# Performance work log

Measured on AMD Instinct MI355X. Metric: run time of the kernel, lower is better.

## Reference

```python
import jax, jax.numpy as jnp
import numpy as np

N_NODES = 100000
N_EDGES = 1200000
HID = 64
N_LAYERS = 3
GAMMA = -0.45
ZETA = 1.05


def setup_inputs() -> dict:
    key = jax.random.key(0)
    ks = jax.random.split(key, 8)
    s = 0.05
    return {
        "features": jax.random.normal(ks[0], (N_NODES, HID), jnp.float32),
        "nb_W": jax.random.normal(ks[1], (N_LAYERS, HID, HID), jnp.float32) * s,
        "nb_b": jnp.zeros((N_LAYERS, HID), jnp.float32),
        "self_W": jax.random.normal(ks[2], (N_LAYERS, HID, HID), jnp.float32) * s,
        "self_b": jnp.zeros((N_LAYERS, HID), jnp.float32),
        "att1_W": jax.random.normal(ks[3], (N_LAYERS, 2 * HID, HID), jnp.float32) * s,
        "att1_b": jnp.zeros((N_LAYERS, HID), jnp.float32),
        "att2_W": jax.random.normal(ks[4], (N_LAYERS, HID, 1), jnp.float32) * s,
        "att2_b": jnp.zeros((N_LAYERS, 1), jnp.float32),
        "row": jax.random.randint(ks[5], (N_EDGES,), 0, N_NODES, jnp.int32),
        "col": jax.random.randint(ks[6], (N_EDGES,), 0, N_NODES, jnp.int32),
    }


def reference(features, nb_W, nb_b, self_W, self_b, att1_W, att1_b, att2_W, att2_b, row, col):
    n = features.shape[0]
    x = features
    out = features  # embedsLst[0]
    for l in range(N_LAYERS):
        # per-edge gather + attention MLPs
        f1 = jax.nn.relu(x[row] @ nb_W[l] + nb_b[l])          # [E, H]
        f2 = jax.nn.relu(x[col] @ self_W[l] + self_b[l])      # [E, H]
        h = jax.nn.relu(jnp.concatenate([f1, f2], axis=1) @ att1_W[l] + att1_b[l])
        log_alpha = (h @ att2_W[l] + att2_b[l])[:, 0]          # [E]
        # hard-concrete gate (deterministic / eval branch)
        mask = jnp.clip(jax.nn.sigmoid(log_alpha) * (ZETA - GAMMA) + GAMMA, 0.0, 1.0)
        # symmetric degree normalization
        rowsum = jax.ops.segment_sum(mask, row, num_segments=n) + 1e-6
        d_inv_sqrt = jnp.clip(rowsum ** -0.5, 0.0, 10.0)
        vals = mask * d_inv_sqrt[row] * d_inv_sqrt[col]        # [E]
        # spmm aggregate: x_new[i] = sum_e vals[e] * x[col[e]] for row[e]==i
        x = jax.ops.segment_sum(vals[:, None] * x[col], row, num_segments=n)
        out = out + x
    return out
```

## Files before the change

kernel.cpp:

```cpp
#include <hip/hip_runtime.h>
#include <hip/hip_bf16.h>
#include <math.h>

#define HID 64
#define BK 8
#define B_WG 256
#define KMAX 512

typedef __attribute__((ext_vector_type(4))) float f32x4;
typedef __attribute__((ext_vector_type(4))) short s16x4;

__device__ __forceinline__ ushort f2b(float x) {
    __hip_bfloat16 h = __float2bfloat16(x);
    return *reinterpret_cast<ushort*>(&h);
}
__device__ __forceinline__ float b2f(ushort u) {
    return __uint_as_float(((unsigned)u) << 16);
}

__device__ __forceinline__ f32x4 mfma16(s16x4 a, s16x4 b, f32x4 c) {
    asm("s_nop 1\n\tv_mfma_f32_16x16x16_bf16 %0, %1, %2, %0"
        : "+v"(c) : "v"(a), "v"(b));
    return c;
}

__global__ __launch_bounds__(256) void cvt_bf16_kernel(const float* __restrict__ x,
                                                       ushort* __restrict__ x16, long n8)
{
    long i = (long)blockIdx.x * 256 + threadIdx.x;
    if (i >= n8) return;
    const float4* s = reinterpret_cast<const float4*>(x) + i * 2;
    float4 a = s[0], b = s[1];
    union { uint4 q; ushort s[8]; } pk;
    pk.s[0] = f2b(a.x); pk.s[1] = f2b(a.y); pk.s[2] = f2b(a.z); pk.s[3] = f2b(a.w);
    pk.s[4] = f2b(b.x); pk.s[5] = f2b(b.y); pk.s[6] = f2b(b.z); pk.s[7] = f2b(b.w);
    reinterpret_cast<uint4*>(x16)[i] = pk.q;
}

template<bool A_FROM_REGS, bool STORE_GLOBAL>
__device__ __forceinline__ void mfma_stage(
    const s16x4 afr[2][4], const ushort (*Wt)[68], const float* bias,
    ushort (*gld)[68], int w, int l, ushort* dstg, int rbase, int n)
{
    f32x4 acc[2][4];
    #pragma unroll
    for (int ct = 0; ct < 4; ++ct) {
        float bv = bias ? bias[(ct << 4) + (l & 15)] : 0.f;
        acc[0][ct] = (f32x4){bv, bv, bv, bv};
        acc[1][ct] = (f32x4){bv, bv, bv, bv};
    }
    #pragma unroll
    for (int kc = 0; kc < 4; ++kc) {
        s16x4 a0, a1;
        if (A_FROM_REGS) {
            a0 = afr[0][kc]; a1 = afr[1][kc];
        } else {
            a0 = *(const s16x4*)&gld[w*32 +  0 + (l & 15)][((l >> 4) << 2) + (kc << 4)];
            a1 = *(const s16x4*)&gld[w*32 + 16 + (l & 15)][((l >> 4) << 2) + (kc << 4)];
        }
        #pragma unroll
        for (int ct = 0; ct < 4; ++ct) {
            s16x4 b = *(const s16x4*)&Wt[(ct << 4) + (l & 15)][((l >> 4) << 2) + (kc << 4)];
            acc[0][ct] = mfma16(a0, b, acc[0][ct]);
            acc[1][ct] = mfma16(a1, b, acc[1][ct]);
        }
    }
    asm volatile("s_nop 7\n\ts_nop 7");
    #pragma unroll
    for (int rt = 0; rt < 2; ++rt)
    #pragma unroll
    for (int ct = 0; ct < 4; ++ct)
    #pragma unroll
    for (int j = 0; j < 4; ++j) {
        int rloc = w*32 + rt*16 + ((l >> 4) << 2) + j;
        if (STORE_GLOBAL) {
            int rg = rbase + rloc;
            if (rg < n)
                dstg[(size_t)rg * HID + (ct << 4) + (l & 15)] = f2b(acc[rt][ct][j]);
        } else {
            gld[rloc][(ct << 4) + (l & 15)] = f2b(fmaxf(acc[rt][ct][j], 0.f));
        }
    }
}

__global__ __launch_bounds__(256) void node_mlp_mfma(
    const ushort* __restrict__ x16,
    const float* __restrict__ W1, const float* __restrict__ b1,
    const float* __restrict__ W2, const float* __restrict__ b2,
    const float* __restrict__ A12,
    const float* __restrict__ ab,
    ushort* __restrict__ u, ushort* __restrict__ v, int n)
{
    __shared__ ushort Wt[4][64][68];
    __shared__ ushort gld[128][68];
    int tid = threadIdx.x;
    int l = tid & 63, w = tid >> 6;
    int rbase = blockIdx.x * 128;

    const float* Wsrc[4] = { W1, A12, W2, A12 + HID*HID };
    for (int m = 0; m < 4; ++m) {
        const float4* s4 = reinterpret_cast<const float4*>(Wsrc[m]);
        #pragma unroll
        for (int q = 0; q < 4; ++q) {
            float4 t = s4[tid*4 + q];
            int idx = tid*16 + q*4;
            int k = idx >> 6, c = idx & 63;
            Wt[m][c+0][k] = f2b(t.x); Wt[m][c+1][k] = f2b(t.y);
            Wt[m][c+2][k] = f2b(t.z); Wt[m][c+3][k] = f2b(t.w);
        }
    }

    s16x4 afr[2][4];
    #pragma unroll
    for (int rt = 0; rt < 2; ++rt) {
        int r = rbase + w*32 + rt*16 + (l & 15);
        int rc = min(r, n - 1);
        const ushort* xr = x16 + (size_t)rc * HID + ((l >> 4) << 2);
        #pragma unroll
        for (int kc = 0; kc < 4; ++kc)
            afr[rt][kc] = *(const s16x4*)(xr + (kc << 4));
    }
    __syncthreads();

    mfma_stage<true,  false>(afr, Wt[0], b1,      gld, w, l, nullptr, rbase, n);
    mfma_stage<false, true >(afr, Wt[1], ab,      gld, w, l, u,       rbase, n);
    mfma_stage<true,  false>(afr, Wt[2], b2,      gld, w, l, nullptr, rbase, n);
    mfma_stage<false, true >(afr, Wt[3], nullptr, gld, w, l, v,       rbase, n);
}

__global__ __launch_bounds__(256) void bucket_hist(const int* __restrict__ row,
                                                   int* __restrict__ hist,
                                                   int E, int K, int chunk)
{
    __shared__ int h[KMAX];
    for (int i = threadIdx.x; i < K; i += 256) h[i] = 0;
    __syncthreads();
    int w = blockIdx.x;
    int s = w * chunk, e = min(E, s + chunk);
    for (int i = s + threadIdx.x; i < e; i += 256)
        atomicAdd(&h[row[i] >> BK], 1);
    __syncthreads();
    for (int i = threadIdx.x; i < K; i += 256)
        hist[i * B_WG + w] = h[i];
}

__global__ __launch_bounds__(512) void bucket_base(const int* __restrict__ hist,
                                                   int* __restrict__ bbase,
                                                   int* __restrict__ ptr,
                                                   int K, int E, int n)
{
    __shared__ int lds[512];
    int t = threadIdx.x;
    int total = 0;
    if (t < K) {
        const int* hrow = hist + t * B_WG;
        for (int w = 0; w < B_WG; ++w) total += hrow[w];
    }
    lds[t] = total;
    __syncthreads();
    int val = total;
    for (int off = 1; off < 512; off <<= 1) {
        int tmp = (t >= off) ? lds[t - off] : 0;
        __syncthreads();
        val += tmp;
        lds[t] = val;
        __syncthreads();
    }
    if (t <= K) bbase[t] = val - total;
    if (t == 0) ptr[n] = E;
}

__global__ __launch_bounds__(B_WG) void wg_offsets(const int* __restrict__ hist,
                                                   const int* __restrict__ bbase,
                                                   int* __restrict__ offs)
{
    __shared__ int lds[B_WG];
    int b = blockIdx.x, t = threadIdx.x;
    int v = hist[b * B_WG + t];
    lds[t] = v;
    __syncthreads();
    int val = v;
    for (int off = 1; off < B_WG; off <<= 1) {
        int tmp = (t >= off) ? lds[t - off] : 0;
        __syncthreads();
        val += tmp;
        lds[t] = val;
        __syncthreads();
    }
    offs[b * B_WG + t] = bbase[b] + val - v;
}

__global__ __launch_bounds__(256) void partition_edges(const int* __restrict__ row,
                                                       const int* __restrict__ col,
                                                       const int* __restrict__ offs,
                                                       int2* __restrict__ tmp,
                                                       int E, int K, int chunk)
{
    __shared__ int cur[KMAX];
    int w = blockIdx.x;
    for (int i = threadIdx.x; i < K; i += 256)
        cur[i] = offs[i * B_WG + w];
    __syncthreads();
    int s = w * chunk, e = min(E, s + chunk);
    for (int i = s + threadIdx.x; i < e; i += 256) {
        int r = row[i], c = col[i];
        int pos = atomicAdd(&cur[r >> BK], 1);
        tmp[pos] = make_int2(r, c);
    }
}

__global__ __launch_bounds__(256) void fine_sort(const int2* __restrict__ tmp,
                                                 const int* __restrict__ bbase,
                                                 int* __restrict__ ptr,
                                                 int* __restrict__ row_sorted,
                                                 int* __restrict__ col_sorted,
                                                 int n)
{
    __shared__ int rcnt[256];
    __shared__ int scan[256];
    __shared__ int cur[256];
    int b = blockIdx.x, t = threadIdx.x;
    int row0 = b << BK;
    rcnt[t] = 0;
    __syncthreads();
    int s = bbase[b], e = bbase[b + 1];
    for (int i = s + t; i < e; i += 256)
        atomicAdd(&rcnt[tmp[i].x & 255], 1);
    __syncthreads();
    int v = rcnt[t];
    scan[t] = v;
    __syncthreads();
    int val = v;
    for (int off = 1; off < 256; off <<= 1) {
        int tm = (t >= off) ? scan[t - off] : 0;
        __syncthreads();
        val += tm;
        scan[t] = val;
        __syncthreads();
    }
    int rstart = s + val - v;
    int r = row0 + t;
    if (r < n) ptr[r] = rstart;
    cur[t] = rstart;
    __syncthreads();
    for (int i = s + t; i < e; i += 256) {
        int2 rc = tmp[i];
        int pos = atomicAdd(&cur[rc.x & 255], 1);
        row_sorted[pos] = rc.x;
        col_sorted[pos] = rc.y;
    }
}

__global__ __launch_bounds__(256) void edge_mask8(
    const ushort* __restrict__ u, const ushort* __restrict__ v,
    const float* __restrict__ w2, const float* __restrict__ b2p,
    const int* __restrict__ rows, const int* __restrict__ cols,
    float* __restrict__ mask_sorted, int E)
{
    int g = (blockIdx.x * 256 + threadIdx.x) >> 3;
    if (g >= E) return;
    int sub = threadIdx.x & 7;
    int r = rows[g], c = cols[g];
    union { uint4 q; ushort s[8]; } uu, vv;
    uu.q = *reinterpret_cast<const uint4*>(u + (size_t)r * HID + sub * 8);
    vv.q = *reinterpret_cast<const uint4*>(v + (size_t)c * HID + sub * 8);
    float4 wa = *reinterpret_cast<const float4*>(w2 + sub * 8);
    float4 wb = *reinterpret_cast<const float4*>(w2 + sub * 8 + 4);
    float p;
    p =        fmaxf(b2f(uu.s[0]) + b2f(vv.s[0]), 0.f) * wa.x;
    p = fmaf(fmaxf(b2f(uu.s[1]) + b2f(vv.s[1]), 0.f), wa.y, p);
    p = fmaf(fmaxf(b2f(uu.s[2]) + b2f(vv.s[2]), 0.f), wa.z, p);
    p = fmaf(fmaxf(b2f(uu.s[3]) + b2f(vv.s[3]), 0.f), wa.w, p);
    p = fmaf(fmaxf(b2f(uu.s[4]) + b2f(vv.s[4]), 0.f), wb.x, p);
    p = fmaf(fmaxf(b2f(uu.s[5]) + b2f(vv.s[5]), 0.f), wb.y, p);
    p = fmaf(fmaxf(b2f(uu.s[6]) + b2f(vv.s[6]), 0.f), wb.z, p);
    p = fmaf(fmaxf(b2f(uu.s[7]) + b2f(vv.s[7]), 0.f), wb.w, p);
    p += __shfl_xor(p, 1, 64);
    p += __shfl_xor(p, 2, 64);
    p += __shfl_xor(p, 4, 64);
    if (sub == 0) {
        float la = p + b2p[0];
        float s = 1.f / (1.f + __expf(-la));
        mask_sorted[g] = fminf(fmaxf(fmaf(s, 1.5f, -0.45f), 0.f), 1.f);
    }
}

__global__ __launch_bounds__(256) void rowsum_dinv(
    const float* __restrict__ mask_sorted, const int* __restrict__ ptr,
    float* __restrict__ dinv, int n)
{
    int i = blockIdx.x * 256 + threadIdx.x;
    if (i >= n) return;
    int s0 = ptr[i], s1 = ptr[i + 1];
    float s = 1e-6f;
    for (int e = s0; e < s1; ++e) s += mask_sorted[e];
    float d = 1.f / sqrtf(s);
    dinv[i] = fminf(d, 10.f);
}

__global__ __launch_bounds__(256) void agg_csr2(
    const ushort* __restrict__ x16,
    const float* __restrict__ mask_sorted, const float* __restrict__ dinv,
    const int* __restrict__ ptr, const int* __restrict__ col_sorted,
    const float* __restrict__ base_in, float* __restrict__ out,
    ushort* __restrict__ x16_out, int n)
{
    int wid = (blockIdx.x * 256 + threadIdx.x) >> 6;
    if (wid >= n) return;
    int lane = threadIdx.x & 63;
    int half = lane >> 5;
    int d2 = lane & 31;
    int start = ptr[wid], end = ptr[wid + 1];
    int deg = end - start;
    float ax = 0.f, ay = 0.f;

    for (int base = 0; base < deg; base += 64) {
        int mcnt = min(64, deg - base);
        int cc = 0; float wv = 0.f;
        if (lane < mcnt) {
            cc = col_sorted[start + base + lane];
            wv = mask_sorted[start + base + lane] * dinv[cc];
        }
        int j = 0;
        for (; j + 8 <= mcnt; j += 8) {
            int jj = j + half;
            int   c0 = __shfl(cc, jj,     64);
            int   c1 = __shfl(cc, jj + 2, 64);
            int   c2 = __shfl(cc, jj + 4, 64);
            int   c3 = __shfl(cc, jj + 6, 64);
            float w0 = __shfl(wv, jj,     64);
            float w1 = __shfl(wv, jj + 2, 64);
            float w2 = __shfl(wv, jj + 4, 64);
            float w3 = __shfl(wv, jj + 6, 64);
            uint p0 = *reinterpret_cast<const uint*>(x16 + (size_t)c0 * HID + d2 * 2);
            uint p1 = *reinterpret_cast<const uint*>(x16 + (size_t)c1 * HID + d2 * 2);
            uint p2 = *reinterpret_cast<const uint*>(x16 + (size_t)c2 * HID + d2 * 2);
            uint p3 = *reinterpret_cast<const uint*>(x16 + (size_t)c3 * HID + d2 * 2);
            ax = fmaf(w0, b2f((ushort)p0), ax); ay = fmaf(w0, b2f((ushort)(p0 >> 16)), ay);
            ax = fmaf(w1, b2f((ushort)p1), ax); ay = fmaf(w1, b2f((ushort)(p1 >> 16)), ay);
            ax = fmaf(w2, b2f((ushort)p2), ax); ay = fmaf(w2, b2f((ushort)(p2 >> 16)), ay);
            ax = fmaf(w3, b2f((ushort)p3), ax); ay = fmaf(w3, b2f((ushort)(p3 >> 16)), ay);
        }
        for (; j < mcnt; j += 2) {
            int jj = j + half;
            int   c0 = __shfl(cc, jj, 64);
            float w0 = __shfl(wv, jj, 64);
            uint p0 = *reinterpret_cast<const uint*>(x16 + (size_t)c0 * HID + d2 * 2);
            ax = fmaf(w0, b2f((ushort)p0), ax);
            ay = fmaf(w0, b2f((ushort)(p0 >> 16)), ay);
        }
    }
    ax += __shfl_xor(ax, 32, 64);
    ay += __shfl_xor(ay, 32, 64);
    if (half == 0) {
        float dv = dinv[wid];
        float rx = ax * dv, ry = ay * dv;
        size_t o2 = (size_t)wid * 32 + d2;
        float2 b = reinterpret_cast<const float2*>(base_in)[o2];
        float2 ov; ov.x = b.x + rx; ov.y = b.y + ry;
        reinterpret_cast<float2*>(out)[o2] = ov;
        uint pk = (uint)f2b(rx) | ((uint)f2b(ry) << 16);
        reinterpret_cast<uint*>(x16_out)[o2] = pk;
    }
}


extern "C" void kernel_launch(void* const* d_in, const int* in_sizes, int n_in,
                              void* d_out, int out_size, void* d_ws, size_t ws_size,
                              hipStream_t stream)
{
    const float* feat  = (const float*)d_in[0];
    const float* nbW   = (const float*)d_in[1];
    const float* nbb   = (const float*)d_in[2];
    const float* selfW = (const float*)d_in[3];
    const float* selfb = (const float*)d_in[4];
    const float* a1W   = (const float*)d_in[5];
    const float* a1b   = (const float*)d_in[6];
    const float* a2W   = (const float*)d_in[7];
    const float* a2b   = (const float*)d_in[8];
    const int*   row   = (const int*)d_in[9];
    const int*   col   = (const int*)d_in[10];
    float* out = (float*)d_out;

    const int n = in_sizes[0] / HID;
    const int E = in_sizes[9];
    const int L = in_sizes[1] / (HID * HID);
    const size_t NH = (size_t)n * HID;
    const int K = (n + 255) >> BK;
    const int chunk = (E + B_WG - 1) / B_WG;

    char* p = (char*)d_ws;
    ushort* u          = (ushort*)p; p += NH * 2;
    ushort* v          = (ushort*)p; p += NH * 2;
    ushort* x16a       = (ushort*)p; p += NH * 2;
    ushort* x16b       = (ushort*)p; p += NH * 2;
    float* dinv        = (float*)p;  p += (size_t)n * 4;
    float* mask_sorted = (float*)p;  p += (size_t)E * 4;
    int*   col_sorted  = (int*)p;    p += (size_t)E * 4;
    int*   row_sorted  = (int*)p;    p += (size_t)E * 4;
    int2*  tmp_rc      = (int2*)p;   p += (size_t)E * 8;
    int*   ptr         = (int*)p;    p += (size_t)(n + 1) * 4;
    int*   hist        = (int*)p;    p += (size_t)KMAX * B_WG * 4;
    int*   offs        = (int*)p;    p += (size_t)KMAX * B_WG * 4;
    int*   bbase       = (int*)p;    p += 1024 * 4;

    const int wBlocks = (int)(((size_t)n * 64 + 255) / 256);
    const int mBlocks = (E + 31) / 32;
    const int nodeBlocks = (n + 127) / 128;

    bucket_hist<<<B_WG, 256, 0, stream>>>(row, hist, E, K, chunk);
    bucket_base<<<1, 512, 0, stream>>>(hist, bbase, ptr, K, E, n);
    wg_offsets<<<K, B_WG, 0, stream>>>(hist, bbase, offs);
    partition_edges<<<B_WG, 256, 0, stream>>>(row, col, offs, tmp_rc, E, K, chunk);
    fine_sort<<<K, 256, 0, stream>>>(tmp_rc, bbase, ptr, row_sorted, col_sorted, n);

    cvt_bf16_kernel<<<(int)((NH / 8 + 255) / 256), 256, 0, stream>>>(feat, x16a, (long)(NH / 8));

    const ushort* x_in = x16a;
    ushort* x_out = x16b;
    for (int l = 0; l < L; ++l) {
        node_mlp_mfma<<<nodeBlocks, 256, 0, stream>>>(
            x_in,
            nbW + (size_t)l * HID * HID,   nbb + (size_t)l * HID,
            selfW + (size_t)l * HID * HID, selfb + (size_t)l * HID,
            a1W + (size_t)l * 2 * HID * HID,
            a1b + (size_t)l * HID,
            u, v, n);

        edge_mask8<<<mBlocks, 256, 0, stream>>>(
            u, v, a2W + (size_t)l * HID, a2b + l,
            row_sorted, col_sorted, mask_sorted, E);

        rowsum_dinv<<<(n + 255) / 256, 256, 0, stream>>>(mask_sorted, ptr, dinv, n);

        agg_csr2<<<wBlocks, 256, 0, stream>>>(
            x_in, mask_sorted, dinv, ptr, col_sorted,
            (l == 0) ? feat : out, out, x_out, n);

        ushort* t = (ushort*)x_in;
        x_in = x_out;
        x_out = (l == 0) ? x16a : t;
    }
}
```

Before: 366.0 us.

## Pack sort scratch, defer residual sum to last layer, unroll gather wider

```diff
diff --git a/kernel.cpp b/kernel.cpp
--- a/kernel.cpp
+++ b/kernel.cpp
@@ -193,7 +193,7 @@
 __global__ __launch_bounds__(256) void partition_edges(const int* __restrict__ row,
                                                        const int* __restrict__ col,
                                                        const int* __restrict__ offs,
-                                                       int2* __restrict__ tmp,
+                                                       uint* __restrict__ tmp,
                                                        int E, int K, int chunk)
 {
     __shared__ int cur[KMAX];
@@ -205,11 +205,11 @@
     for (int i = s + threadIdx.x; i < e; i += 256) {
         int r = row[i], c = col[i];
         int pos = atomicAdd(&cur[r >> BK], 1);
-        tmp[pos] = make_int2(r, c);
-    }
-}
-
-__global__ __launch_bounds__(256) void fine_sort(const int2* __restrict__ tmp,
+        tmp[pos] = ((uint)(r & 255) << 24) | (uint)c;
+    }
+}
+
+__global__ __launch_bounds__(256) void fine_sort(const uint* __restrict__ tmp,
                                                  const int* __restrict__ bbase,
                                                  int* __restrict__ ptr,
                                                  int* __restrict__ row_sorted,
@@ -225,7 +225,7 @@
     __syncthreads();
     int s = bbase[b], e = bbase[b + 1];
     for (int i = s + t; i < e; i += 256)
-        atomicAdd(&rcnt[tmp[i].x & 255], 1);
+        atomicAdd(&rcnt[tmp[i] >> 24], 1);
     __syncthreads();
     int v = rcnt[t];
     scan[t] = v;
@@ -244,10 +244,10 @@
     cur[t] = rstart;
     __syncthreads();
     for (int i = s + t; i < e; i += 256) {
-        int2 rc = tmp[i];
-        int pos = atomicAdd(&cur[rc.x & 255], 1);
-        row_sorted[pos] = rc.x;
-        col_sorted[pos] = rc.y;
+        uint rc = tmp[i];
+        int pos = atomicAdd(&cur[rc >> 24], 1);
+        row_sorted[pos] = row0 | (int)(rc >> 24);
+        col_sorted[pos] = (int)(rc & 0xFFFFFFu);
     }
 }
 
@@ -298,12 +298,14 @@
     dinv[i] = fminf(d, 10.f);
 }
 
+template<bool LAST>
 __global__ __launch_bounds__(256) void agg_csr2(
     const ushort* __restrict__ x16,
     const float* __restrict__ mask_sorted, const float* __restrict__ dinv,
     const int* __restrict__ ptr, const int* __restrict__ col_sorted,
-    const float* __restrict__ base_in, float* __restrict__ out,
-    ushort* __restrict__ x16_out, int n)
+    ushort* __restrict__ x16_out,
+    const float* __restrict__ feat, const ushort* __restrict__ r1,
+    const ushort* __restrict__ r2, float* __restrict__ out, int n)
 {
     int wid = (blockIdx.x * 256 + threadIdx.x) >> 6;
     if (wid >= n) return;
@@ -312,6 +314,7 @@
     int d2 = lane & 31;
     int start = ptr[wid], end = ptr[wid + 1];
     int deg = end - start;
+    const ushort* xb = x16 + d2 * 2;
     float ax = 0.f, ay = 0.f;
 
     for (int base = 0; base < deg; base += 64) {
@@ -321,33 +324,41 @@
             cc = col_sorted[start + base + lane];
             wv = mask_sorted[start + base + lane] * dinv[cc];
         }
-        int j = 0;
-        for (; j + 8 <= mcnt; j += 8) {
+        int m16 = (mcnt + 15) & ~15;
+        for (int j = 0; j < m16; j += 16) {
             int jj = j + half;
-            int   c0 = __shfl(cc, jj,     64);
-            int   c1 = __shfl(cc, jj + 2, 64);
-            int   c2 = __shfl(cc, jj + 4, 64);
-            int   c3 = __shfl(cc, jj + 6, 64);
-            float w0 = __shfl(wv, jj,     64);
-            float w1 = __shfl(wv, jj + 2, 64);
-            float w2 = __shfl(wv, jj + 4, 64);
-            float w3 = __shfl(wv, jj + 6, 64);
-            uint p0 = *reinterpret_cast<const uint*>(x16 + (size_t)c0 * HID + d2 * 2);
-            uint p1 = *reinterpret_cast<const uint*>(x16 + (size_t)c1 * HID + d2 * 2);
-            uint p2 = *reinterpret_cast<const uint*>(x16 + (size_t)c2 * HID + d2 * 2);
-            uint p3 = *reinterpret_cast<const uint*>(x16 + (size_t)c3 * HID + d2 * 2);
+            int   c0 = __shfl(cc, jj,      64);
+            int   c1 = __shfl(cc, jj + 2,  64);
+            int   c2 = __shfl(cc, jj + 4,  64);
+            int   c3 = __shfl(cc, jj + 6,  64);
+            int   c4 = __shfl(cc, jj + 8,  64);
+            int   c5 = __shfl(cc, jj + 10, 64);
+            int   c6 = __shfl(cc, jj + 12, 64);
+            int   c7 = __shfl(cc, jj + 14, 64);
+            float w0 = __shfl(wv, jj,      64);
+            float w1 = __shfl(wv, jj + 2,  64);
+            float w2 = __shfl(wv, jj + 4,  64);
+            float w3 = __shfl(wv, jj + 6,  64);
+            float w4 = __shfl(wv, jj + 8,  64);
+            float w5 = __shfl(wv, jj + 10, 64);
+            float w6 = __shfl(wv, jj + 12, 64);
+            float w7 = __shfl(wv, jj + 14, 64);
+            uint p0 = *reinterpret_cast<const uint*>(xb + (size_t)c0 * HID);
+            uint p1 = *reinterpret_cast<const uint*>(xb + (size_t)c1 * HID);
+            uint p2 = *reinterpret_cast<const uint*>(xb + (size_t)c2 * HID);
+            uint p3 = *reinterpret_cast<const uint*>(xb + (size_t)c3 * HID);
+            uint p4 = *reinterpret_cast<const uint*>(xb + (size_t)c4 * HID);
+            uint p5 = *reinterpret_cast<const uint*>(xb + (size_t)c5 * HID);
+            uint p6 = *reinterpret_cast<const uint*>(xb + (size_t)c6 * HID);
+            uint p7 = *reinterpret_cast<const uint*>(xb + (size_t)c7 * HID);
             ax = fmaf(w0, b2f((ushort)p0), ax); ay = fmaf(w0, b2f((ushort)(p0 >> 16)), ay);
             ax = fmaf(w1, b2f((ushort)p1), ax); ay = fmaf(w1, b2f((ushort)(p1 >> 16)), ay);
             ax = fmaf(w2, b2f((ushort)p2), ax); ay = fmaf(w2, b2f((ushort)(p2 >> 16)), ay);
             ax = fmaf(w3, b2f((ushort)p3), ax); ay = fmaf(w3, b2f((ushort)(p3 >> 16)), ay);
-        }
-        for (; j < mcnt; j += 2) {
-            int jj = j + half;
-            int   c0 = __shfl(cc, jj, 64);
-            float w0 = __shfl(wv, jj, 64);
-            uint p0 = *reinterpret_cast<const uint*>(x16 + (size_t)c0 * HID + d2 * 2);
-            ax = fmaf(w0, b2f((ushort)p0), ax);
-            ay = fmaf(w0, b2f((ushort)(p0 >> 16)), ay);
+            ax = fmaf(w4, b2f((ushort)p4), ax); ay = fmaf(w4, b2f((ushort)(p4 >> 16)), ay);
+            ax = fmaf(w5, b2f((ushort)p5), ax); ay = fmaf(w5, b2f((ushort)(p5 >> 16)), ay);
+            ax = fmaf(w6, b2f((ushort)p6), ax); ay = fmaf(w6, b2f((ushort)(p6 >> 16)), ay);
+            ax = fmaf(w7, b2f((ushort)p7), ax); ay = fmaf(w7, b2f((ushort)(p7 >> 16)), ay);
         }
     }
     ax += __shfl_xor(ax, 32, 64);
@@ -356,11 +367,18 @@
         float dv = dinv[wid];
         float rx = ax * dv, ry = ay * dv;
         size_t o2 = (size_t)wid * 32 + d2;
-        float2 b = reinterpret_cast<const float2*>(base_in)[o2];
-        float2 ov; ov.x = b.x + rx; ov.y = b.y + ry;
-        reinterpret_cast<float2*>(out)[o2] = ov;
-        uint pk = (uint)f2b(rx) | ((uint)f2b(ry) << 16);
-        reinterpret_cast<uint*>(x16_out)[o2] = pk;
+        if (LAST) {
+            float2 f = reinterpret_cast<const float2*>(feat)[o2];
+            uint a1 = reinterpret_cast<const uint*>(r1)[o2];
+            uint a2 = reinterpret_cast<const uint*>(r2)[o2];
+            float2 o;
+            o.x = f.x + b2f((ushort)a1) + b2f((ushort)a2) + rx;
+            o.y = f.y + b2f((ushort)(a1 >> 16)) + b2f((ushort)(a2 >> 16)) + ry;
+            reinterpret_cast<float2*>(out)[o2] = o;
+        } else {
+            uint pk = (uint)f2b(rx) | ((uint)f2b(ry) << 16);
+            reinterpret_cast<uint*>(x16_out)[o2] = pk;
+        }
     }
 }
 
@@ -392,13 +410,14 @@
     char* p = (char*)d_ws;
     ushort* u          = (ushort*)p; p += NH * 2;
     ushort* v          = (ushort*)p; p += NH * 2;
-    ushort* x16a       = (ushort*)p; p += NH * 2;
-    ushort* x16b       = (ushort*)p; p += NH * 2;
+    ushort* xf         = (ushort*)p; p += NH * 2;
+    ushort* r1         = (ushort*)p; p += NH * 2;
+    ushort* r2         = (ushort*)p; p += NH * 2;
     float* dinv        = (float*)p;  p += (size_t)n * 4;
     float* mask_sorted = (float*)p;  p += (size_t)E * 4;
     int*   col_sorted  = (int*)p;    p += (size_t)E * 4;
     int*   row_sorted  = (int*)p;    p += (size_t)E * 4;
-    int2*  tmp_rc      = (int2*)p;   p += (size_t)E * 8;
+    uint*  tmp_rc      = (uint*)p;   p += (size_t)E * 4;
     int*   ptr         = (int*)p;    p += (size_t)(n + 1) * 4;
     int*   hist        = (int*)p;    p += (size_t)KMAX * B_WG * 4;
     int*   offs        = (int*)p;    p += (size_t)KMAX * B_WG * 4;
@@ -414,10 +433,10 @@
     partition_edges<<<B_WG, 256, 0, stream>>>(row, col, offs, tmp_rc, E, K, chunk);
     fine_sort<<<K, 256, 0, stream>>>(tmp_rc, bbase, ptr, row_sorted, col_sorted, n);
 
-    cvt_bf16_kernel<<<(int)((NH / 8 + 255) / 256), 256, 0, stream>>>(feat, x16a, (long)(NH / 8));
-
-    const ushort* x_in = x16a;
-    ushort* x_out = x16b;
+    cvt_bf16_kernel<<<(int)((NH / 8 + 255) / 256), 256, 0, stream>>>(feat, xf, (long)(NH / 8));
+
+    ushort* res[2] = { r1, r2 };
+    const ushort* x_in = xf;
     for (int l = 0; l < L; ++l) {
         node_mlp_mfma<<<nodeBlocks, 256, 0, stream>>>(
             x_in,
@@ -433,12 +452,15 @@
 
         rowsum_dinv<<<(n + 255) / 256, 256, 0, stream>>>(mask_sorted, ptr, dinv, n);
 
-        agg_csr2<<<wBlocks, 256, 0, stream>>>(
-            x_in, mask_sorted, dinv, ptr, col_sorted,
-            (l == 0) ? feat : out, out, x_out, n);
-
-        ushort* t = (ushort*)x_in;
-        x_in = x_out;
-        x_out = (l == 0) ? x16a : t;
-    }
-}
+        if (l == L - 1) {
+            agg_csr2<true><<<wBlocks, 256, 0, stream>>>(
+                x_in, mask_sorted, dinv, ptr, col_sorted,
+                nullptr, feat, r1, r2, out, n);
+        } else {
+            agg_csr2<false><<<wBlocks, 256, 0, stream>>>(
+                x_in, mask_sorted, dinv, ptr, col_sorted,
+                res[l], nullptr, nullptr, nullptr, nullptr, n);
+            x_in = res[l];
+        }
+    }
+}
```

Measured after the change: 340.3 us. -7.0%, faster.
